# Kernel optimization log

Hardware: AMD Instinct MI355X
Metric: run time of the kernel (lower is better)

The kernel has to match this reference:

```python
import jax, jax.numpy as jnp
import numpy as np

NC = 80          # num classes (len(yolov8.names))
CONF = 0.25      # ultralytics conf_thres default
IOU_T = 0.45     # ultralytics iou_thres default
MAX_DET = 300    # module default max_det
K = 1024         # pre-NMS candidate cap (static stand-in for max_nms)
MAX_WH = 7680.0  # ultralytics class-offset for multi-class NMS


def setup_inputs() -> dict:
    key = jax.random.key(0)
    k1, k2, k3 = jax.random.split(key, 3)
    B, A = 32, 8400
    # YOLOv8 head layout: rows 0:4 = xywh (pixels), rows 4: = sigmoid class scores
    xy = jax.random.uniform(k1, (B, 2, A), dtype=jnp.float32) * 640.0
    wh = jax.random.uniform(k2, (B, 2, A), dtype=jnp.float32) * 160.0 + 8.0
    scores = jax.random.uniform(k3, (B, NC, A), dtype=jnp.float32) ** 3  # mostly below conf_thres
    preds = jnp.concatenate([xy, wh, scores], axis=1)  # [B, 4+NC, A]
    return {"preds": preds}


def _box_iou(b):
    # b: [K, 4] xyxy -> [K, K] pairwise IoU
    area = (b[:, 2] - b[:, 0]) * (b[:, 3] - b[:, 1])
    lt = jnp.maximum(b[:, None, :2], b[None, :, :2])
    rb = jnp.minimum(b[:, None, 2:], b[None, :, 2:])
    wh = jnp.clip(rb - lt, 0.0)
    inter = wh[..., 0] * wh[..., 1]
    return inter / (area[:, None] + area[None, :] - inter + 1e-7)


def _nms_single(pred):
    # pred: [4+NC, A]
    boxes_xywh = pred[:4].T           # [A, 4]
    cls_scores = pred[4:].T           # [A, NC]
    conf = cls_scores.max(-1)         # best-class confidence per anchor
    cls = jnp.argmax(cls_scores, -1)
    score = jnp.where(conf > CONF, conf, 0.0)
    top, idx = jax.lax.top_k(score, K)            # K candidates by confidence
    xywh = boxes_xywh[idx]
    half = xywh[:, 2:] * 0.5
    boxes = jnp.concatenate([xywh[:, :2] - half, xywh[:, :2] + half], -1)  # xyxy
    cls_k = cls[idx]
    valid = top > CONF
    # multi-class NMS via per-class coordinate offset (ultralytics trick)
    iou = _box_iou(boxes + (cls_k.astype(boxes.dtype) * MAX_WH)[:, None])
    ar = jnp.arange(K)

    def body(i, st):
        supp, keep = st
        ki = valid[i] & ~supp[i]
        keep = keep.at[i].set(ki)
        supp = supp | (ki & (iou[i] > IOU_T) & (ar > i))
        return supp, keep

    _, keep = jax.lax.fori_loop(0, K, body,
                                (jnp.zeros(K, bool), jnp.zeros(K, bool)))
    fscore = jnp.where(keep, top, 0.0)
    sc, order = jax.lax.top_k(fscore, MAX_DET)
    det = jnp.concatenate(
        [boxes[order], top[order][:, None], cls_k[order].astype(boxes.dtype)[:, None]], -1)
    # pad invalid rows with value NC in every column (matches F.pad(value=len(names)))
    return jnp.where((sc > CONF)[:, None], det, jnp.float32(NC))


def reference(preds):
    # [B, MAX_DET, 6] -> (x1, y1, x2, y2, conf, cls), padded rows filled with NC
    return jax.vmap(_nms_single)(preds)
```

## Files before the change

kernel.cpp:

```cpp
#include <hip/hip_runtime.h>
#include <stdint.h>

typedef unsigned long long u64;
typedef unsigned int u32;

#define NC 80
#define CONF_T 0.25f
#define IOU_THR 0.45f
#define MAX_DET 300
#define KCAND 1024
#define A_ANCH 8400
#define NROWS 84
#define MAX_WH 7680.0f

__global__ void yolo_conf_kernel(const float* __restrict__ preds, u64* __restrict__ keys) {
    int b = blockIdx.x / 9;
    int chunk = blockIdx.x % 9;
    int g = chunk * 256 + threadIdx.x;
    if (g >= A_ANCH / 4) return;
    int a0 = g * 4;
    const float* base = preds + ((size_t)b * NROWS + 4) * A_ANCH + a0;
    float4 best = *(const float4*)base;
    int bcx = 0, bcy = 0, bcz = 0, bcw = 0;
#pragma unroll 4
    for (int c = 1; c < NC; ++c) {
        float4 v = *(const float4*)(base + (size_t)c * A_ANCH);
        if (v.x > best.x) { best.x = v.x; bcx = c; }
        if (v.y > best.y) { best.y = v.y; bcy = c; }
        if (v.z > best.z) { best.z = v.z; bcz = c; }
        if (v.w > best.w) { best.w = v.w; bcw = c; }
    }
    u64* ko = keys + (size_t)b * A_ANCH + a0;
    float bs[4] = {best.x, best.y, best.z, best.w};
    int bc[4] = {bcx, bcy, bcz, bcw};
#pragma unroll
    for (int q = 0; q < 4; ++q) {
        float score = (bs[q] > CONF_T) ? bs[q] : 0.0f;
        u32 bits = __float_as_uint(score);
        ko[q] = ((u64)bits << 32) | ((u64)(16383 - (a0 + q)) << 7) | (u64)bc[q];
    }
}

__device__ __forceinline__ float iou_f(float ix1, float iy1, float ix2, float iy2, float iar,
                                       float jx1, float jy1, float jx2, float jy2, float jar) {
    float lx = fmaxf(ix1, jx1), ly = fmaxf(iy1, jy1);
    float rx = fminf(ix2, jx2), ry = fminf(iy2, jy2);
    float ww = fmaxf(__fsub_rn(rx, lx), 0.0f);
    float hh = fmaxf(__fsub_rn(ry, ly), 0.0f);
    float inter = __fmul_rn(ww, hh);
    float den = __fadd_rn(__fsub_rn(__fadd_rn(iar, jar), inter), 1e-7f);
    return __fdiv_rn(inter, den);
}

__global__ __launch_bounds__(1024) void yolo_nms_kernel(const float* __restrict__ preds,
                                                        const u64* __restrict__ keys,
                                                        float* __restrict__ out) {
    const int b = blockIdx.x;
    const int tid = threadIdx.x;
    const int lane = tid & 63;
    const int wid = tid >> 6;

    __shared__ u32 sc[A_ANCH];
    __shared__ u64 skey[KCAND];
    __shared__ u32 histw[16][256];
    __shared__ u32 hist[256];
    __shared__ union {
        struct { u32 eqw[264]; u32 wpre[264]; } pre;
        struct { u64 rows[64]; int keptlist[384]; } post;
    } ov;
    __shared__ u32 s_scal[4];
    __shared__ u32 s_csupp[2];
    __shared__ u32 s_nkept;

    const u64* kb = keys + (size_t)b * A_ANCH;
    for (int a = tid; a < A_ANCH; a += 1024) sc[a] = (u32)(kb[a] >> 32);
    if (tid == 0) { s_scal[0] = 0; s_scal[1] = KCAND; s_scal[2] = 0; s_csupp[0] = 0; s_csupp[1] = 0; s_nkept = 0; }
    __syncthreads();

    for (int p = 0; p < 4; ++p) {
        int shift = 24 - 8 * p;
        u32* hwf = &histw[0][0];
        for (int i = tid; i < 16 * 256; i += 1024) hwf[i] = 0;
        __syncthreads();
        u32 prefix = s_scal[0];
#pragma unroll
        for (int it = 0; it < 9; ++it) {
            int a = tid + it * 1024;
            u32 v = 0, bin = 0;
            bool m = false;
            if (a < A_ANCH) {
                v = sc[a];
                m = (p == 0) || ((v >> (shift + 8)) == prefix);
                bin = (v >> shift) & 255u;
            }
            u64 actm = __ballot(m);
            if (actm) {
                int fl = __ffsll(actm) - 1;
                u32 fb = __shfl(bin, fl);
                if (__ballot(m && (bin != fb)) == 0ull) {
                    if (lane == fl) atomicAdd(&histw[wid][fb], (u32)__popcll(actm));
                } else if (m) {
                    atomicAdd(&histw[wid][bin], 1u);
                }
            }
        }
        __syncthreads();
        if (tid < 256) {
            u32 s = 0;
#pragma unroll
            for (int w = 0; w < 16; ++w) s += histw[w][tid];
            hist[tid] = s;
        }
        __syncthreads();
        if (wid == 0) {
            u32 g[4], loc = 0;
#pragma unroll
            for (int q = 0; q < 4; ++q) { g[q] = hist[255 - (lane * 4 + q)]; loc += g[q]; }
            u32 pre = loc;
#pragma unroll
            for (int off = 1; off < 64; off <<= 1) {
                u32 o = __shfl_up(pre, off);
                if (lane >= off) pre += o;
            }
            u32 run = pre - loc;
            u32 rem = s_scal[1];
            u32 pfx = s_scal[0];
#pragma unroll
            for (int q = 0; q < 4; ++q) {
                int d = 255 - (lane * 4 + q);
                if (run < rem && rem <= run + g[q]) {
                    s_scal[0] = (pfx << 8) | (u32)d;
                    s_scal[1] = rem - run;
                }
                run += g[q];
            }
        }
        __syncthreads();
    }
    const u32 P = s_scal[0];
    const u32 tEq = s_scal[1];

    if (tid < 264) ov.pre.eqw[tid] = 0;
    __syncthreads();
    for (int a = tid; a < A_ANCH; a += 1024)
        if (sc[a] == P) atomicOr(&ov.pre.eqw[a >> 5], 1u << (a & 31));
    __syncthreads();
    if (wid == 0) {
        u32 cnt[5], loc = 0;
#pragma unroll
        for (int q = 0; q < 5; ++q) {
            int w2 = lane * 5 + q;
            u32 e = (w2 < 264) ? ov.pre.eqw[w2] : 0u;
            cnt[q] = (u32)__popc(e); loc += cnt[q];
        }
        u32 pre = loc;
#pragma unroll
        for (int off = 1; off < 64; off <<= 1) {
            u32 o = __shfl_up(pre, off);
            if (lane >= off) pre += o;
        }
        u32 run = pre - loc;
#pragma unroll
        for (int q = 0; q < 5; ++q) {
            int w2 = lane * 5 + q;
            if (w2 < 264) ov.pre.wpre[w2] = run;
            run += cnt[q];
        }
    }
    __syncthreads();

    for (int a = tid; a < A_ANCH; a += 1024) {
        u32 v = sc[a];
        bool take = v > P;
        if (!take && v == P) {
            u32 r = ov.pre.wpre[a >> 5] + (u32)__popc(ov.pre.eqw[a >> 5] & ((1u << (a & 31)) - 1u));
            take = (r < tEq);
        }
        if (take) {
            u32 pos = atomicAdd(&s_scal[2], 1u);
            skey[pos] = kb[a];
        }
    }
    __syncthreads();

    for (u32 size = 2; size <= KCAND; size <<= 1) {
        for (u32 stride = size >> 1; stride >= 1; stride >>= 1) {
            __syncthreads();
            if (tid < KCAND / 2) {
                u32 i1 = ((u32)(tid & ~(int)(stride - 1)) << 1) | ((u32)tid & (stride - 1));
                u32 i2 = i1 + stride;
                bool descSeg = ((i1 & size) == 0);
                u64 x = skey[i1], y = skey[i2];
                if ((x < y) == descSeg) { skey[i1] = y; skey[i2] = x; }
            }
        }
    }
    __syncthreads();

    float* BX1 = (float*)sc;
    float* BY1 = BX1 + KCAND;
    float* BX2 = BX1 + 2 * KCAND;
    float* BY2 = BX1 + 3 * KCAND;
    float* BAR = BX1 + 4 * KCAND;
    {
        u64 key = skey[tid];
        int cls = (int)(key & 127u);
        int idx = 16383 - (int)((key >> 7) & 16383u);
        const float* pb = preds + (size_t)b * NROWS * A_ANCH + idx;
        float x = pb[0];
        float y = pb[A_ANCH];
        float w = pb[2 * A_ANCH];
        float h = pb[3 * A_ANCH];
        float hw = __fmul_rn(w, 0.5f), hh = __fmul_rn(h, 0.5f);
        float x1 = __fsub_rn(x, hw), x2 = __fadd_rn(x, hw);
        float y1 = __fsub_rn(y, hh), y2 = __fadd_rn(y, hh);
        float off = __fmul_rn((float)cls, MAX_WH);
        float bx1 = __fadd_rn(x1, off), bx2 = __fadd_rn(x2, off);
        float by1 = __fadd_rn(y1, off), by2 = __fadd_rn(y2, off);
        BX1[tid] = bx1; BY1[tid] = by1; BX2[tid] = bx2; BY2[tid] = by2;
        BAR[tid] = __fmul_rn(__fsub_rn(bx2, bx1), __fsub_rn(by2, by1));
    }
    __syncthreads();

    for (int c = 0; c < KCAND / 64; ++c) {
        int j = c * 64 + lane;
        u64 keyj = skey[j];
        float scj = __uint_as_float((u32)(keyj >> 32));
        float jx1 = BX1[j], jy1 = BY1[j], jx2 = BX2[j], jy2 = BY2[j], jar = BAR[j];

        u32 nk = s_nkept;
        u32 suppbit = 0;
        for (u32 k = wid; k < nk; k += 16) {
            int i = ov.post.keptlist[k];
            if (iou_f(BX1[i], BY1[i], BX2[i], BY2[i], BAR[i], jx1, jy1, jx2, jy2, jar) > IOU_THR) {
                suppbit = 1; break;
            }
        }
        u64 bm = __ballot(suppbit != 0);
        if (lane == 0 && bm) {
            atomicOr(&s_csupp[0], (u32)bm);
            atomicOr(&s_csupp[1], (u32)(bm >> 32));
        }

#pragma unroll
        for (int p2 = 0; p2 < 4; ++p2) {
            int i = p2 * 16 + wid;
            int ci = c * 64 + i;
            float iou = iou_f(BX1[ci], BY1[ci], BX2[ci], BY2[ci], BAR[ci], jx1, jy1, jx2, jy2, jar);
            u64 m = __ballot((lane > i) && (iou > IOU_THR));
            if (lane == 0) ov.post.rows[i] = m;
        }
        __syncthreads();

        if (wid == 0) {
            u64 row = ov.post.rows[lane];
            u64 csupp = (((u64)s_csupp[1]) << 32) | (u64)s_csupp[0];
            u64 valid = __ballot(scj > CONF_T) & ~csupp;
            u32 rlo = (u32)row, rhi = (u32)(row >> 32);
            u64 supp = 0, keep = 0;
#pragma unroll
            for (int i = 0; i < 64; ++i) {
                u64 ri = (((u64)__shfl(rhi, i)) << 32) | (u64)__shfl(rlo, i);
                bool ki = (((valid & ~supp) >> i) & 1ull) != 0;
                if (ki) { keep |= (1ull << i); supp |= ri; }
            }
            u32 base = s_nkept;
            if ((keep >> lane) & 1ull) {
                u32 r = (u32)__popcll(keep & ((1ull << lane) - 1ull));
                ov.post.keptlist[base + r] = j;
            }
            if (lane == 0) {
                s_nkept = base + (u32)__popcll(keep);
                s_csupp[0] = 0; s_csupp[1] = 0;
            }
        }
        __syncthreads();
        if (s_nkept >= MAX_DET) break;
    }

    if (tid < MAX_DET) {
        u32 nk = s_nkept;
        float row[6];
        int t = (tid < (int)(nk < MAX_DET ? nk : MAX_DET)) ? ov.post.keptlist[tid] : -1;
        if (t >= 0) {
            u64 key = skey[t];
            u32 bits = (u32)(key >> 32);
            float score = __uint_as_float(bits);
            int cls = (int)(key & 127u);
            int idx = 16383 - (int)((key >> 7) & 16383u);
            const float* pb = preds + (size_t)b * NROWS * A_ANCH + idx;
            float x = pb[0], y = pb[A_ANCH], w = pb[2 * A_ANCH], h = pb[3 * A_ANCH];
            float hw = __fmul_rn(w, 0.5f), hh = __fmul_rn(h, 0.5f);
            row[0] = __fsub_rn(x, hw);
            row[1] = __fsub_rn(y, hh);
            row[2] = __fadd_rn(x, hw);
            row[3] = __fadd_rn(y, hh);
            row[4] = score;
            row[5] = (float)cls;
        } else {
            row[0] = row[1] = row[2] = row[3] = row[4] = row[5] = (float)NC;
        }
        float* o = out + ((size_t)b * MAX_DET + tid) * 6;
#pragma unroll
        for (int q = 0; q < 6; ++q) o[q] = row[q];
    }
}

extern "C" void kernel_launch(void* const* d_in, const int* in_sizes, int n_in,
                              void* d_out, int out_size, void* d_ws, size_t ws_size,
                              hipStream_t stream) {
    const float* preds = (const float*)d_in[0];
    float* out = (float*)d_out;
    u64* keys = (u64*)d_ws;
    int B = in_sizes[0] / (NROWS * A_ANCH);
    yolo_conf_kernel<<<dim3(B * 9), dim3(256), 0, stream>>>(preds, keys);
    yolo_nms_kernel<<<dim3(B), dim3(1024), 0, stream>>>(preds, keys, out);
}
```

Before: 80.44 us.

## Rework NMS kernel: 512 threads, register bitonic sort, class-filtered IoU, cached kept boxes

The conf kernel now has each thread handle two anchors with float2 loads and one 16-byte key store, in 512-thread blocks. The NMS kernel drops to 512 threads and keeps the score values in registers so the first histogram pass skips shared memory. The per-wave histograms are padded to 257 entries. The bitonic sort runs its small strides inside a wavefront with shuffles instead of shared memory and barriers. NMS skips IoU computation when no lane shares a class, keeps a compact copy of kept-box coordinates and classes in shared memory, and uses readlane for the greedy scan. These changes trade fewer barriers and less shared-memory traffic for fewer threads per batch block, which may lengthen the serial parts.

```diff
diff --git a/kernel.cpp b/kernel.cpp
--- a/kernel.cpp
+++ b/kernel.cpp
@@ -13,32 +13,27 @@
 #define NROWS 84
 #define MAX_WH 7680.0f
 
-__global__ void yolo_conf_kernel(const float* __restrict__ preds, u64* __restrict__ keys) {
+__global__ __launch_bounds__(512) void yolo_conf_kernel(const float* __restrict__ preds,
+                                                        u64* __restrict__ keys) {
     int b = blockIdx.x / 9;
-    int chunk = blockIdx.x % 9;
-    int g = chunk * 256 + threadIdx.x;
-    if (g >= A_ANCH / 4) return;
-    int a0 = g * 4;
+    int g = (blockIdx.x % 9) * 512 + threadIdx.x;
+    if (g >= A_ANCH / 2) return;
+    int a0 = g * 2;
     const float* base = preds + ((size_t)b * NROWS + 4) * A_ANCH + a0;
-    float4 best = *(const float4*)base;
-    int bcx = 0, bcy = 0, bcz = 0, bcw = 0;
-#pragma unroll 4
+    float2 best = *(const float2*)base;
+    int bc0 = 0, bc1 = 0;
+#pragma unroll 8
     for (int c = 1; c < NC; ++c) {
-        float4 v = *(const float4*)(base + (size_t)c * A_ANCH);
-        if (v.x > best.x) { best.x = v.x; bcx = c; }
-        if (v.y > best.y) { best.y = v.y; bcy = c; }
-        if (v.z > best.z) { best.z = v.z; bcz = c; }
-        if (v.w > best.w) { best.w = v.w; bcw = c; }
-    }
-    u64* ko = keys + (size_t)b * A_ANCH + a0;
-    float bs[4] = {best.x, best.y, best.z, best.w};
-    int bc[4] = {bcx, bcy, bcz, bcw};
-#pragma unroll
-    for (int q = 0; q < 4; ++q) {
-        float score = (bs[q] > CONF_T) ? bs[q] : 0.0f;
-        u32 bits = __float_as_uint(score);
-        ko[q] = ((u64)bits << 32) | ((u64)(16383 - (a0 + q)) << 7) | (u64)bc[q];
-    }
+        float2 v = *(const float2*)(base + (size_t)c * A_ANCH);
+        if (v.x > best.x) { best.x = v.x; bc0 = c; }
+        if (v.y > best.y) { best.y = v.y; bc1 = c; }
+    }
+    float s0 = (best.x > CONF_T) ? best.x : 0.0f;
+    float s1 = (best.y > CONF_T) ? best.y : 0.0f;
+    ulonglong2 kk;
+    kk.x = ((u64)__float_as_uint(s0) << 32) | ((u64)(16383 - a0) << 7) | (u64)bc0;
+    kk.y = ((u64)__float_as_uint(s1) << 32) | ((u64)(16383 - (a0 + 1)) << 7) | (u64)bc1;
+    *(ulonglong2*)(keys + (size_t)b * A_ANCH + a0) = kk;
 }
 
 __device__ __forceinline__ float iou_f(float ix1, float iy1, float ix2, float iy2, float iar,
@@ -52,9 +47,25 @@
     return __fdiv_rn(inter, den);
 }
 
-__global__ __launch_bounds__(1024) void yolo_nms_kernel(const float* __restrict__ preds,
-                                                        const u64* __restrict__ keys,
-                                                        float* __restrict__ out) {
+__device__ __forceinline__ void hadd(u32* h, u32 bin, bool m, int lane) {
+    u64 act = __ballot(m);
+    if (act == 0) return;
+    int fl = __ffsll((unsigned long long)act) - 1;
+    u32 fb = __shfl(bin, fl);
+    u64 same = __ballot(m && (bin == fb));
+    if (lane == fl) atomicAdd(&h[fb], (u32)__popcll(same));
+    if (m && (bin != fb)) atomicAdd(&h[bin], 1u);
+}
+
+__device__ __forceinline__ u64 bstep(u64 v, u32 idx, u32 size, u32 stride) {
+    u64 v2 = __shfl_xor((unsigned long long)v, (int)stride, 64);
+    bool keep_big = (((idx & stride) == 0) == ((idx & size) == 0));
+    return ((v > v2) == keep_big) ? v : v2;
+}
+
+__global__ __launch_bounds__(512) void yolo_nms_kernel(const float* __restrict__ preds,
+                                                       const u64* __restrict__ keys,
+                                                       float* __restrict__ out) {
     const int b = blockIdx.x;
     const int tid = threadIdx.x;
     const int lane = tid & 63;
@@ -62,53 +73,65 @@
 
     __shared__ u32 sc[A_ANCH];
     __shared__ u64 skey[KCAND];
-    __shared__ u32 histw[16][256];
+    __shared__ u32 histw[8 * 257];
     __shared__ u32 hist[256];
-    __shared__ union {
+    union OvU {
         struct { u32 eqw[264]; u32 wpre[264]; } pre;
-        struct { u64 rows[64]; int keptlist[384]; } post;
-    } ov;
+        struct {
+            u64 rows[64];
+            int keptlist[364];
+            float kx1[364], ky1[364], kx2[364], ky2[364], kar[364];
+            u32 kcls[364];
+        } post;
+    };
+    __shared__ OvU ov;
     __shared__ u32 s_scal[4];
     __shared__ u32 s_csupp[2];
     __shared__ u32 s_nkept;
 
     const u64* kb = keys + (size_t)b * A_ANCH;
-    for (int a = tid; a < A_ANCH; a += 1024) sc[a] = (u32)(kb[a] >> 32);
+
+    for (int i = tid; i < 8 * 257; i += 512) histw[i] = 0;
     if (tid == 0) { s_scal[0] = 0; s_scal[1] = KCAND; s_scal[2] = 0; s_csupp[0] = 0; s_csupp[1] = 0; s_nkept = 0; }
-    __syncthreads();
-
+
+    u32 vals[17];
+#pragma unroll
+    for (int it = 0; it < 17; ++it) {
+        int a = tid + it * 512;
+        vals[it] = (a < A_ANCH) ? (u32)(kb[a] >> 32) : 0u;
+    }
+#pragma unroll
+    for (int it = 0; it < 17; ++it) {
+        int a = tid + it * 512;
+        if (a < A_ANCH) sc[a] = vals[it];
+    }
+    __syncthreads();
+
+    u32* hw = histw + wid * 257;
     for (int p = 0; p < 4; ++p) {
-        int shift = 24 - 8 * p;
-        u32* hwf = &histw[0][0];
-        for (int i = tid; i < 16 * 256; i += 1024) hwf[i] = 0;
-        __syncthreads();
-        u32 prefix = s_scal[0];
-#pragma unroll
-        for (int it = 0; it < 9; ++it) {
-            int a = tid + it * 1024;
-            u32 v = 0, bin = 0;
-            bool m = false;
-            if (a < A_ANCH) {
-                v = sc[a];
-                m = (p == 0) || ((v >> (shift + 8)) == prefix);
-                bin = (v >> shift) & 255u;
-            }
-            u64 actm = __ballot(m);
-            if (actm) {
-                int fl = __ffsll(actm) - 1;
-                u32 fb = __shfl(bin, fl);
-                if (__ballot(m && (bin != fb)) == 0ull) {
-                    if (lane == fl) atomicAdd(&histw[wid][fb], (u32)__popcll(actm));
-                } else if (m) {
-                    atomicAdd(&histw[wid][bin], 1u);
-                }
+        if (p == 0) {
+#pragma unroll
+            for (int it = 0; it < 17; ++it) {
+                int a = tid + it * 512;
+                hadd(hw, vals[it] >> 24, a < A_ANCH, lane);
+            }
+        } else {
+            for (int i = tid; i < 8 * 257; i += 512) histw[i] = 0;
+            __syncthreads();
+            u32 prefix = s_scal[0];
+            int shift = 24 - 8 * p;
+            for (int it = 0; it < 17; ++it) {
+                int a = tid + it * 512;
+                u32 v = (a < A_ANCH) ? sc[a] : 0u;
+                bool m = (a < A_ANCH) && ((v >> (shift + 8)) == prefix);
+                hadd(hw, (v >> shift) & 255u, m, lane);
             }
         }
         __syncthreads();
         if (tid < 256) {
             u32 s = 0;
 #pragma unroll
-            for (int w = 0; w < 16; ++w) s += histw[w][tid];
+            for (int w = 0; w < 8; ++w) s += histw[w * 257 + tid];
             hist[tid] = s;
         }
         __syncthreads();
@@ -142,8 +165,10 @@
 
     if (tid < 264) ov.pre.eqw[tid] = 0;
     __syncthreads();
-    for (int a = tid; a < A_ANCH; a += 1024)
-        if (sc[a] == P) atomicOr(&ov.pre.eqw[a >> 5], 1u << (a & 31));
+    for (int it = 0; it < 17; ++it) {
+        int a = tid + it * 512;
+        if (a < A_ANCH && sc[a] == P) atomicOr(&ov.pre.eqw[a >> 5], 1u << (a & 31));
+    }
     __syncthreads();
     if (wid == 0) {
         u32 cnt[5], loc = 0;
@@ -169,41 +194,65 @@
     }
     __syncthreads();
 
-    for (int a = tid; a < A_ANCH; a += 1024) {
-        u32 v = sc[a];
-        bool take = v > P;
-        if (!take && v == P) {
-            u32 r = ov.pre.wpre[a >> 5] + (u32)__popc(ov.pre.eqw[a >> 5] & ((1u << (a & 31)) - 1u));
-            take = (r < tEq);
-        }
-        if (take) {
-            u32 pos = atomicAdd(&s_scal[2], 1u);
-            skey[pos] = kb[a];
-        }
-    }
-    __syncthreads();
-
-    for (u32 size = 2; size <= KCAND; size <<= 1) {
-        for (u32 stride = size >> 1; stride >= 1; stride >>= 1) {
+    for (int it = 0; it < 17; ++it) {
+        int a = tid + it * 512;
+        if (a < A_ANCH) {
+            u32 v = sc[a];
+            bool take = v > P;
+            if (!take && v == P) {
+                u32 r = ov.pre.wpre[a >> 5] + (u32)__popc(ov.pre.eqw[a >> 5] & ((1u << (a & 31)) - 1u));
+                take = (r < tEq);
+            }
+            if (take) {
+                u32 pos = atomicAdd(&s_scal[2], 1u);
+                skey[pos] = kb[a];
+            }
+        }
+    }
+    __syncthreads();
+
+    {
+        u64 vA = skey[tid], vB = skey[tid + 512];
+        const u32 iA = (u32)tid, iB = (u32)tid + 512;
+#pragma unroll
+        for (u32 size = 2; size <= 64; size <<= 1) {
+#pragma unroll
+            for (u32 stride = size >> 1; stride >= 1; stride >>= 1) {
+                vA = bstep(vA, iA, size, stride);
+                vB = bstep(vB, iB, size, stride);
+            }
+        }
+        skey[tid] = vA; skey[tid + 512] = vB;
+        __syncthreads();
+        for (u32 size = 128; size <= 1024; size <<= 1) {
+            for (u32 stride = size >> 1; stride >= 64; stride >>= 1) {
+                u32 i1 = ((tid & ~(int)(stride - 1)) << 1) | (tid & (stride - 1));
+                u32 i2 = i1 + stride;
+                bool desc = ((i1 & size) == 0);
+                u64 x = skey[i1], y = skey[i2];
+                if ((x < y) == desc) { skey[i1] = y; skey[i2] = x; }
+                __syncthreads();
+            }
+            vA = skey[tid]; vB = skey[tid + 512];
+#pragma unroll
+            for (u32 stride = 32; stride >= 1; stride >>= 1) {
+                vA = bstep(vA, iA, size, stride);
+                vB = bstep(vB, iB, size, stride);
+            }
+            skey[tid] = vA; skey[tid + 512] = vB;
             __syncthreads();
-            if (tid < KCAND / 2) {
-                u32 i1 = ((u32)(tid & ~(int)(stride - 1)) << 1) | ((u32)tid & (stride - 1));
-                u32 i2 = i1 + stride;
-                bool descSeg = ((i1 & size) == 0);
-                u64 x = skey[i1], y = skey[i2];
-                if ((x < y) == descSeg) { skey[i1] = y; skey[i2] = x; }
-            }
-        }
-    }
-    __syncthreads();
+        }
+    }
 
     float* BX1 = (float*)sc;
     float* BY1 = BX1 + KCAND;
     float* BX2 = BX1 + 2 * KCAND;
     float* BY2 = BX1 + 3 * KCAND;
     float* BAR = BX1 + 4 * KCAND;
-    {
-        u64 key = skey[tid];
+#pragma unroll
+    for (int q = 0; q < 2; ++q) {
+        int t = tid + q * 512;
+        u64 key = skey[t];
         int cls = (int)(key & 127u);
         int idx = 16383 - (int)((key >> 7) & 16383u);
         const float* pb = preds + (size_t)b * NROWS * A_ANCH + idx;
@@ -217,8 +266,8 @@
         float off = __fmul_rn((float)cls, MAX_WH);
         float bx1 = __fadd_rn(x1, off), bx2 = __fadd_rn(x2, off);
         float by1 = __fadd_rn(y1, off), by2 = __fadd_rn(y2, off);
-        BX1[tid] = bx1; BY1[tid] = by1; BX2[tid] = bx2; BY2[tid] = by2;
-        BAR[tid] = __fmul_rn(__fsub_rn(bx2, bx1), __fsub_rn(by2, by1));
+        BX1[t] = bx1; BY1[t] = by1; BX2[t] = bx2; BY2[t] = by2;
+        BAR[t] = __fmul_rn(__fsub_rn(bx2, bx1), __fsub_rn(by2, by1));
     }
     __syncthreads();
 
@@ -226,48 +275,60 @@
         int j = c * 64 + lane;
         u64 keyj = skey[j];
         float scj = __uint_as_float((u32)(keyj >> 32));
+        u32 clsj = (u32)(keyj & 127u);
         float jx1 = BX1[j], jy1 = BY1[j], jx2 = BX2[j], jy2 = BY2[j], jar = BAR[j];
 
         u32 nk = s_nkept;
-        u32 suppbit = 0;
-        for (u32 k = wid; k < nk; k += 16) {
-            int i = ov.post.keptlist[k];
-            if (iou_f(BX1[i], BY1[i], BX2[i], BY2[i], BAR[i], jx1, jy1, jx2, jy2, jar) > IOU_THR) {
-                suppbit = 1; break;
-            }
-        }
-        u64 bm = __ballot(suppbit != 0);
-        if (lane == 0 && bm) {
+        bool suppbit = false;
+        for (u32 k = wid; k < nk; k += 8) {
+            bool cm = (ov.post.kcls[k] == clsj);
+            if (__ballot(cm)) {
+                float iou = iou_f(ov.post.kx1[k], ov.post.ky1[k], ov.post.kx2[k], ov.post.ky2[k],
+                                  ov.post.kar[k], jx1, jy1, jx2, jy2, jar);
+                suppbit |= (cm && (iou > IOU_THR));
+            }
+        }
+        u64 bm = __ballot(suppbit);
+        if (bm && lane == 0) {
             atomicOr(&s_csupp[0], (u32)bm);
             atomicOr(&s_csupp[1], (u32)(bm >> 32));
         }
 
 #pragma unroll
-        for (int p2 = 0; p2 < 4; ++p2) {
-            int i = p2 * 16 + wid;
+        for (int p2 = 0; p2 < 8; ++p2) {
+            int i = p2 * 8 + wid;
             int ci = c * 64 + i;
-            float iou = iou_f(BX1[ci], BY1[ci], BX2[ci], BY2[ci], BAR[ci], jx1, jy1, jx2, jy2, jar);
-            u64 m = __ballot((lane > i) && (iou > IOU_THR));
+            u32 clsi = (u32)(skey[ci] & 127u);
+            u64 m = 0;
+            if (__ballot(clsi == clsj)) {
+                float iou = iou_f(BX1[ci], BY1[ci], BX2[ci], BY2[ci], BAR[ci],
+                                  jx1, jy1, jx2, jy2, jar);
+                m = __ballot((lane > i) && (iou > IOU_THR));
+            }
             if (lane == 0) ov.post.rows[i] = m;
         }
         __syncthreads();
 
         if (wid == 0) {
             u64 row = ov.post.rows[lane];
+            u32 rlo = (u32)row, rhi = (u32)(row >> 32);
             u64 csupp = (((u64)s_csupp[1]) << 32) | (u64)s_csupp[0];
             u64 valid = __ballot(scj > CONF_T) & ~csupp;
-            u32 rlo = (u32)row, rhi = (u32)(row >> 32);
             u64 supp = 0, keep = 0;
 #pragma unroll
             for (int i = 0; i < 64; ++i) {
-                u64 ri = (((u64)__shfl(rhi, i)) << 32) | (u64)__shfl(rlo, i);
+                u64 ri = (((u64)(u32)__builtin_amdgcn_readlane((int)rhi, i)) << 32) |
+                         (u64)(u32)__builtin_amdgcn_readlane((int)rlo, i);
                 bool ki = (((valid & ~supp) >> i) & 1ull) != 0;
                 if (ki) { keep |= (1ull << i); supp |= ri; }
             }
             u32 base = s_nkept;
             if ((keep >> lane) & 1ull) {
-                u32 r = (u32)__popcll(keep & ((1ull << lane) - 1ull));
-                ov.post.keptlist[base + r] = j;
+                u32 slot = base + (u32)__popcll(keep & ((1ull << lane) - 1ull));
+                ov.post.keptlist[slot] = j;
+                ov.post.kx1[slot] = jx1; ov.post.ky1[slot] = jy1;
+                ov.post.kx2[slot] = jx2; ov.post.ky2[slot] = jy2;
+                ov.post.kar[slot] = jar; ov.post.kcls[slot] = clsj;
             }
             if (lane == 0) {
                 s_nkept = base + (u32)__popcll(keep);
@@ -284,8 +345,7 @@
         int t = (tid < (int)(nk < MAX_DET ? nk : MAX_DET)) ? ov.post.keptlist[tid] : -1;
         if (t >= 0) {
             u64 key = skey[t];
-            u32 bits = (u32)(key >> 32);
-            float score = __uint_as_float(bits);
+            float score = __uint_as_float((u32)(key >> 32));
             int cls = (int)(key & 127u);
             int idx = 16383 - (int)((key >> 7) & 16383u);
             const float* pb = preds + (size_t)b * NROWS * A_ANCH + idx;
@@ -313,6 +373,6 @@
     float* out = (float*)d_out;
     u64* keys = (u64*)d_ws;
     int B = in_sizes[0] / (NROWS * A_ANCH);
-    yolo_conf_kernel<<<dim3(B * 9), dim3(256), 0, stream>>>(preds, keys);
-    yolo_nms_kernel<<<dim3(B), dim3(1024), 0, stream>>>(preds, keys, out);
-}
+    yolo_conf_kernel<<<dim3(B * 9), dim3(512), 0, stream>>>(preds, keys);
+    yolo_nms_kernel<<<dim3(B), dim3(512), 0, stream>>>(preds, keys, out);
+}
```

Result: no change. 79.15 us (-1.6%).
